# Kernel optimization log

Measured on AMD Instinct MI355X. Metric: run time of the kernel, lower is better.

Reference implementation:

```python
import jax, jax.numpy as jnp
import numpy as np

NUM_REL = 20000
NUM_EDGES = 640000
DIM_IN = 128
DIM_OUT = 128
NUM_HEAD = 8
DIM_HID = DIM_OUT // NUM_HEAD
NUM_BIN = 10
NEG_SLOPE = 0.2


def leaky_relu(x):
    return jnp.where(x >= 0, x, NEG_SLOPE * x)


def setup_inputs() -> dict:
    key = jax.random.key(0)
    ks = jax.random.split(key, 8)
    emb_rel = jax.random.normal(ks[0], (NUM_REL, DIM_IN), dtype=jnp.float32)
    head = jax.random.randint(ks[1], (NUM_EDGES, 1), 0, NUM_REL)
    tail = jax.random.randint(ks[2], (NUM_EDGES, 1), 0, NUM_REL)
    bins = jax.random.randint(ks[3], (NUM_EDGES, 1), 0, NUM_BIN)
    relation_triplets = jnp.concatenate([head, tail, bins], axis=-1).astype(jnp.int64)
    # xavier-normal-ish init
    attn_proj_w = jax.random.normal(ks[4], (DIM_OUT, 2 * DIM_IN), dtype=jnp.float32) * (2.0 / np.sqrt(2 * DIM_IN + DIM_OUT))
    attn_proj_b = jnp.zeros((DIM_OUT,), dtype=jnp.float32)
    attn_bin = jax.random.normal(ks[5], (NUM_BIN, NUM_HEAD, 1), dtype=jnp.float32) * 0.3
    attn_vec = jax.random.normal(ks[6], (1, NUM_HEAD, DIM_HID), dtype=jnp.float32) * (2.0 / np.sqrt(NUM_HEAD * DIM_HID))
    aggr_proj_w = jax.random.normal(ks[7], (DIM_OUT, DIM_IN), dtype=jnp.float32) * (2.0 / np.sqrt(DIM_IN + DIM_OUT))
    aggr_proj_b = jnp.zeros((DIM_OUT,), dtype=jnp.float32)
    return {"emb_rel": emb_rel, "relation_triplets": relation_triplets,
            "attn_proj_w": attn_proj_w, "attn_proj_b": attn_proj_b,
            "attn_bin": attn_bin, "attn_vec": attn_vec,
            "aggr_proj_w": aggr_proj_w, "aggr_proj_b": aggr_proj_b}


def reference(emb_rel, relation_triplets, attn_proj_w, attn_proj_b, attn_bin, attn_vec, aggr_proj_w, aggr_proj_b):
    num_rel = emb_rel.shape[0]
    head = relation_triplets[..., 0]
    tail = relation_triplets[..., 1]
    bins = relation_triplets[..., 2]
    # edge gather + concat: [E, 2*dim_in]
    concat = jnp.concatenate([emb_rel[head], emb_rel[tail]], axis=-1)
    proj = concat @ attn_proj_w.T + attn_proj_b  # [E, dim_out]
    proj = leaky_relu(proj).reshape(-1, NUM_HEAD, DIM_HID)
    attn_raw = (proj * attn_vec).sum(axis=-1, keepdims=True) + leaky_relu(attn_bin[bins])  # [E,H,1]
    # per-head-relation segment softmax over edges grouped by head index
    seg_max = jax.ops.segment_max(attn_raw, head, num_segments=num_rel)  # [R,H,1]
    attn_val = jnp.exp(attn_raw - seg_max[head])
    seg_sum = jax.ops.segment_sum(attn_val, head, num_segments=num_rel)  # [R,H,1]
    beta = attn_val / (seg_sum[head] + 1e-16)
    msg = (emb_rel[tail] @ aggr_proj_w.T + aggr_proj_b).reshape(-1, NUM_HEAD, DIM_HID)
    out = jax.ops.segment_sum(beta * msg, head, num_segments=num_rel)  # [R,H,Dh]
    return out.reshape(num_rel, -1)
```

## Files before the change

kernel.cpp:

```cpp
#include <hip/hip_runtime.h>
#include <hip/hip_bf16.h>
#include <cstdint>
#include <cstddef>

#define NUM_REL    20000
#define NUM_EDGES  640000
#define DIM        128
#define NUM_HEAD   8
#define DIM_HID    16
#define NUM_BIN    10
#define CAP        128
#define CNT_STR    16
#define PROJ_BLKS  471
#define SC_BLKS    1250

using u16 = unsigned short;
using u32 = unsigned int;
typedef __attribute__((ext_vector_type(8))) short bf16x8;
typedef __attribute__((ext_vector_type(4))) float f32x4;

__device__ __forceinline__ float b2f(u16 u) { return __uint_as_float(((u32)u) << 16); }
__device__ __forceinline__ float lo2f(u32 u) { return __uint_as_float(u << 16); }
__device__ __forceinline__ float hi2f(u32 u) { return __uint_as_float(u & 0xffff0000u); }
__device__ __forceinline__ float lrelu(float x) { return fmaxf(x, 0.2f * x); }
__device__ __forceinline__ int clampi(int v, int hi) { return v < 0 ? 0 : (v > hi ? hi : v); }
__device__ __forceinline__ float ldf(const void* p, int f32m, int i)
{ return f32m ? ((const float*)p)[i] : b2f(((const u16*)p)[i]); }
__device__ __forceinline__ u16 f2b(float x)
{ u32 u = __float_as_uint(x); u += 0x7fffu + ((u >> 16) & 1u); return (u16)(u >> 16); }
__device__ __forceinline__ u32 pk2(float a, float b)
{ return (u32)f2b(a) | ((u32)f2b(b) << 16); }

__device__ __forceinline__ void detect_flags(const int* __restrict__ trip,
                                             const u16* __restrict__ emb,
                                             int* sF, int tid)
{
    if (tid < 64) {
        bool odd_zero = (trip[2 * tid + 1] == 0) && (trip[2 * tid + 129] == 0);
        unsigned long long m1 = __ballot(odd_zero);
        int ex = (emb[2 * tid] >> 7) & 0xFF;
        bool inr = (ex >= 110) && (ex <= 136);
        unsigned long long m2 = __ballot(inr);
        if (tid == 0) {
            sF[0] = (~m1 == 0ull) ? 1 : 0;
            sF[1] = (__popcll(m2) >= 32) ? 0 : 1;
        }
    }
    __syncthreads();
}

__global__ __launch_bounds__(256) void k_projscatter(
    const void* __restrict__ emb, const int* __restrict__ trip,
    const void* __restrict__ w_attn, const void* __restrict__ w_aggr,
    const void* __restrict__ b_attn, const void* __restrict__ b_aggr,
    float* __restrict__ A, u16* __restrict__ Bb, u16* __restrict__ Mb,
    int* __restrict__ cnt, int* __restrict__ bucket)
{
    __shared__ u16 sW[128 * 64];
    __shared__ float sBias[128];
    __shared__ int sF[2];

    const int tid = threadIdx.x;
    detect_flags(trip, (const u16*)emb, sF, tid);
    const int is64 = sF[0], f32m = sF[1];

    if (blockIdx.x >= PROJ_BLKS) {
        int e0 = (blockIdx.x - PROJ_BLKS) * 512 + tid;
        int e1 = e0 + 256;
        int h0, t0, b0, h1, t1, b1;
        if (is64) {
            int2 ha = *(const int2*)(trip + 6 * e0);
            int2 ta = *(const int2*)(trip + 6 * e0 + 2);
            int2 ba = *(const int2*)(trip + 6 * e0 + 4);
            int2 hb = *(const int2*)(trip + 6 * e1);
            int2 tb = *(const int2*)(trip + 6 * e1 + 2);
            int2 bb = *(const int2*)(trip + 6 * e1 + 4);
            h0 = ha.x; t0 = ta.x; b0 = ba.x;
            h1 = hb.x; t1 = tb.x; b1 = bb.x;
        } else {
            h0 = trip[3 * e0]; t0 = trip[3 * e0 + 1]; b0 = trip[3 * e0 + 2];
            h1 = trip[3 * e1]; t1 = trip[3 * e1 + 1]; b1 = trip[3 * e1 + 2];
        }
        h0 = clampi(h0, NUM_REL - 1); t0 = clampi(t0, NUM_REL - 1); b0 = clampi(b0, NUM_BIN - 1);
        h1 = clampi(h1, NUM_REL - 1); t1 = clampi(t1, NUM_REL - 1); b1 = clampi(b1, NUM_BIN - 1);
        int p0 = atomicAdd(&cnt[h0 * CNT_STR], 1);
        int p1 = atomicAdd(&cnt[h1 * CNT_STR], 1);
        if (p0 < CAP) bucket[h0 * CAP + p0] = t0 | (b0 << 20);
        if (p1 < CAP) bucket[h1 * CAP + p1] = t1 | (b1 << 20);
        return;
    }

    const int mt = blockIdx.x / 3, nt = blockIdx.x % 3;
    const int r0 = mt * 128;

    if (tid < 128)
        sBias[tid] = (nt == 0) ? 0.f : ldf((nt == 1) ? b_attn : b_aggr, f32m, tid);

    const void* wsrc = (nt == 2) ? w_aggr : w_attn;
    const int stride = (nt == 2) ? 128 : 256;
    const int koff   = (nt == 1) ? 128 : 0;

    const int lane = tid & 63, wid = tid >> 6;
    const int wm = (wid >> 1) * 64, wn = (wid & 1) * 64;
    const int ln15 = lane & 15, q = lane >> 4;

    int arow[4];
    #pragma unroll
    for (int mi = 0; mi < 4; ++mi) {
        int g = r0 + wm + mi * 16 + ln15;
        arow[mi] = (g < NUM_REL) ? g : (NUM_REL - 1);
    }

    f32x4 acc[4][4] = {};
    #pragma unroll
    for (int kh = 0; kh < 2; ++kh) {
        if (kh) __syncthreads();
        if (f32m) {
            const float* src = (const float*)wsrc;
            #pragma unroll
            for (int i = 0; i < 8; ++i) {
                int f = i * 256 + tid;
                int row = f >> 4, pos = f & 15;
                const float* rp = src + (size_t)row * stride + koff + kh * 64;
                float4 x = ((const float4*)rp)[pos];
                int chunk = (pos >> 1) ^ (row & 7);
                *(uint2*)&sW[row * 64 + chunk * 8 + (pos & 1) * 4] =
                    make_uint2(pk2(x.x, x.y), pk2(x.z, x.w));
            }
        } else {
            const u16* src = (const u16*)wsrc;
            #pragma unroll
            for (int i = 0; i < 4; ++i) {
                int f = i * 256 + tid;
                int row = f >> 3, pos = f & 7;
                const u16* rp = src + (size_t)row * stride + koff + kh * 64;
                uint4 x = ((const uint4*)rp)[pos];
                int chunk = pos ^ (row & 7);
                *(uint4*)&sW[row * 64 + chunk * 8] = x;
            }
        }
        __syncthreads();

        #pragma unroll
        for (int k2 = 0; k2 < 2; ++k2) {
            const int kkg = kh * 2 + k2;
            const int kc = (kkg * 4 + q) * 8;
            const int cl = (k2 * 4 + q) ^ (ln15 & 7);
            bf16x8 a[4], b[4];
            #pragma unroll
            for (int mi = 0; mi < 4; ++mi) {
                if (f32m) {
                    const float* er = (const float*)emb + (size_t)arow[mi] * DIM + kc;
                    float4 x0 = *(const float4*)er;
                    float4 x1 = *(const float4*)(er + 4);
                    union { bf16x8 v; u32 u[4]; } cv;
                    cv.u[0] = pk2(x0.x, x0.y); cv.u[1] = pk2(x0.z, x0.w);
                    cv.u[2] = pk2(x1.x, x1.y); cv.u[3] = pk2(x1.z, x1.w);
                    a[mi] = cv.v;
                } else {
                    a[mi] = *(const bf16x8*)((const u16*)emb + (size_t)arow[mi] * DIM + kc);
                }
            }
            #pragma unroll
            for (int ni = 0; ni < 4; ++ni) {
                int n = wn + ni * 16 + ln15;
                b[ni] = *(const bf16x8*)&sW[n * 64 + cl * 8];
            }
            #pragma unroll
            for (int mi = 0; mi < 4; ++mi)
                #pragma unroll
                for (int ni = 0; ni < 4; ++ni)
                    acc[mi][ni] = __builtin_amdgcn_mfma_f32_16x16x32_bf16(
                        a[mi], b[ni], acc[mi][ni], 0, 0, 0);
        }
    }

    #pragma unroll
    for (int mi = 0; mi < 4; ++mi) {
        #pragma unroll
        for (int reg = 0; reg < 4; ++reg) {
            int g = r0 + wm + mi * 16 + q * 4 + reg;
            if (g < NUM_REL) {
                #pragma unroll
                for (int ni = 0; ni < 4; ++ni) {
                    int c = wn + ni * 16 + ln15;
                    float v = acc[mi][ni][reg] + sBias[c];
                    size_t o = (size_t)g * DIM + c;
                    if (nt == 0)      A[o]  = v;
                    else if (nt == 1) Bb[o] = f2b(v);
                    else              Mb[o] = f2b(v);
                }
            }
        }
    }
}

__global__ __launch_bounds__(256, 4) void k_segment(
    const float* __restrict__ A, const u16* __restrict__ Bb,
    const u16* __restrict__ Mb, const void* __restrict__ attn_bin,
    const void* __restrict__ attn_vec, const int* __restrict__ cnt,
    const int* __restrict__ bucket, const int* __restrict__ trip,
    const void* __restrict__ emb, void* __restrict__ out)
{
    __shared__ float sAr[4][DIM];
    __shared__ float sVec[DIM];
    __shared__ float sBin[NUM_BIN * NUM_HEAD];
    __shared__ int sF[2];

    const int tid  = threadIdx.x;
    detect_flags(trip, (const u16*)emb, sF, tid);
    const int f32m = sF[1];

    const int wid  = tid >> 6, lane = tid & 63;
    const int r = blockIdx.x * 4 + wid;
    int nE = cnt[r * CNT_STR]; if (nE > CAP) nE = CAP;
    const int* __restrict__ bk = bucket + r * CAP;

    {
        const float2* ap = (const float2*)(A + (size_t)r * DIM);
        float2 a2 = ap[lane];
        sAr[wid][2 * lane] = a2.x; sAr[wid][2 * lane + 1] = a2.y;
    }
    if (tid < DIM) sVec[tid] = ldf(attn_vec, f32m, tid);
    else if (tid < DIM + NUM_BIN * NUM_HEAD)
        sBin[tid - DIM] = lrelu(ldf(attn_bin, f32m, tid - DIM));
    __syncthreads();

    if (nE == 0) {
        if (f32m) ((float2*)out)[(size_t)r * 64 + lane] = make_float2(0.f, 0.f);
        else      ((u32*)out)[(size_t)r * 64 + lane] = 0;
        return;
    }

    const int el = lane >> 3, hd = lane & 7;
    const int ah = lane >> 3;

    float av[16], vv[16];
    {
        const float4* pA = (const float4*)(&sAr[wid][hd * DIM_HID]);
        const float4* pV = (const float4*)(&sVec[hd * DIM_HID]);
        #pragma unroll
        for (int i = 0; i < 4; ++i) {
            float4 a4 = pA[i], v4 = pV[i];
            av[4*i+0]=a4.x; av[4*i+1]=a4.y; av[4*i+2]=a4.z; av[4*i+3]=a4.w;
            vv[4*i+0]=v4.x; vv[4*i+1]=v4.y; vv[4*i+2]=v4.z; vv[4*i+3]=v4.w;
        }
    }

    const u16* __restrict__ Mbl = Mb + 2 * lane;

    int tba = (el      < nE) ? bk[el]     : 0;
    int tbb = (8 + el  < nE) ? bk[8 + el] : 0;
    int ia = tba & 0xFFFFF, ib = tbb & 0xFFFFF;
    uint4 q0a, q1a, q0b, q1b;
    {
        const uint4* Ba = (const uint4*)(Bb + (size_t)ia * DIM) + hd * 2;
        const uint4* Bc = (const uint4*)(Bb + (size_t)ib * DIM) + hd * 2;
        q0a = Ba[0]; q1a = Ba[1];
        q0b = Bc[0]; q1b = Bc[1];
    }

    float l = 0.f;
    float ax0 = 0.f, ax1 = 0.f, ay0 = 0.f, ay1 = 0.f;

    for (int base = 0; base < nE; base += 16) {
        u32 mm[16];
        #pragma unroll
        for (int k = 0; k < 8; ++k) {
            int tk = __shfl(ia, k * 8);
            mm[k] = *(const u32*)(Mbl + (size_t)tk * DIM);
        }
        #pragma unroll
        for (int k = 0; k < 8; ++k) {
            int tk = __shfl(ib, k * 8);
            mm[8 + k] = *(const u32*)(Mbl + (size_t)tk * DIM);
        }
        const int bsa = (tba >> 20) & 0xF;
        const int bsb = (tbb >> 20) & 0xF;

        int ea_n  = base + 16 + el;
        int eb_n  = base + 24 + el;
        int tba_n = (ea_n < nE) ? bk[ea_n] : 0;
        int tbb_n = (eb_n < nE) ? bk[eb_n] : 0;
        int ia_n  = tba_n & 0xFFFFF, ib_n = tbb_n & 0xFFFFF;
        uint4 q0an, q1an, q0bn, q1bn;
        {
            const uint4* Ban = (const uint4*)(Bb + (size_t)ia_n * DIM) + hd * 2;
            const uint4* Bcn = (const uint4*)(Bb + (size_t)ib_n * DIM) + hd * 2;
            q0an = Ban[0]; q1an = Ban[1];
            q0bn = Bcn[0]; q1bn = Bcn[1];
        }

        float sa0 = sBin[bsa * NUM_HEAD + hd];
        float sb0 = sBin[bsb * NUM_HEAD + hd];
        sa0 = fmaf(lrelu(av[0]  + lo2f(q0a.x)), vv[0],  sa0);
        sb0 = fmaf(lrelu(av[0]  + lo2f(q0b.x)), vv[0],  sb0);
        float sa1 = lrelu(av[1] + hi2f(q0a.x)) * vv[1];
        float sb1 = lrelu(av[1] + hi2f(q0b.x)) * vv[1];
        float sa2 = lrelu(av[2] + lo2f(q0a.y)) * vv[2];
        float sb2 = lrelu(av[2] + lo2f(q0b.y)) * vv[2];
        float sa3 = lrelu(av[3] + hi2f(q0a.y)) * vv[3];
        float sb3 = lrelu(av[3] + hi2f(q0b.y)) * vv[3];
        sa0 = fmaf(lrelu(av[4]  + lo2f(q0a.z)), vv[4],  sa0);
        sb0 = fmaf(lrelu(av[4]  + lo2f(q0b.z)), vv[4],  sb0);
        sa1 = fmaf(lrelu(av[5]  + hi2f(q0a.z)), vv[5],  sa1);
        sb1 = fmaf(lrelu(av[5]  + hi2f(q0b.z)), vv[5],  sb1);
        sa2 = fmaf(lrelu(av[6]  + lo2f(q0a.w)), vv[6],  sa2);
        sb2 = fmaf(lrelu(av[6]  + lo2f(q0b.w)), vv[6],  sb2);
        sa3 = fmaf(lrelu(av[7]  + hi2f(q0a.w)), vv[7],  sa3);
        sb3 = fmaf(lrelu(av[7]  + hi2f(q0b.w)), vv[7],  sb3);
        sa0 = fmaf(lrelu(av[8]  + lo2f(q1a.x)), vv[8],  sa0);
        sb0 = fmaf(lrelu(av[8]  + lo2f(q1b.x)), vv[8],  sb0);
        sa1 = fmaf(lrelu(av[9]  + hi2f(q1a.x)), vv[9],  sa1);
        sb1 = fmaf(lrelu(av[9]  + hi2f(q1b.x)), vv[9],  sb1);
        sa2 = fmaf(lrelu(av[10] + lo2f(q1a.y)), vv[10], sa2);
        sb2 = fmaf(lrelu(av[10] + lo2f(q1b.y)), vv[10], sb2);
        sa3 = fmaf(lrelu(av[11] + hi2f(q1a.y)), vv[11], sa3);
        sb3 = fmaf(lrelu(av[11] + hi2f(q1b.y)), vv[11], sb3);
        sa0 = fmaf(lrelu(av[12] + lo2f(q1a.z)), vv[12], sa0);
        sb0 = fmaf(lrelu(av[12] + lo2f(q1b.z)), vv[12], sb0);
        sa1 = fmaf(lrelu(av[13] + hi2f(q1a.z)), vv[13], sa1);
        sb1 = fmaf(lrelu(av[13] + hi2f(q1b.z)), vv[13], sb1);
        sa2 = fmaf(lrelu(av[14] + lo2f(q1a.w)), vv[14], sa2);
        sb2 = fmaf(lrelu(av[14] + lo2f(q1b.w)), vv[14], sb2);
        sa3 = fmaf(lrelu(av[15] + hi2f(q1a.w)), vv[15], sa3);
        sb3 = fmaf(lrelu(av[15] + hi2f(q1b.w)), vv[15], sb3);
        float sa = (sa0 + sa1) + (sa2 + sa3);
        float sb = (sb0 + sb1) + (sb2 + sb3);
        sa = fminf(fmaxf(sa, -60.f), 60.f);
        sb = fminf(fmaxf(sb, -60.f), 60.f);
        float pa = ((base + el)     < nE) ? __expf(sa) : 0.f;
        float pb = ((base + 8 + el) < nE) ? __expf(sb) : 0.f;
        l += pa + pb;

        #pragma unroll
        for (int k = 0; k < 8; ++k) {
            float v = __shfl(pa, k * 8 + ah);
            if (k & 1) { ax1 = fmaf(v, lo2f(mm[k]), ax1); ay1 = fmaf(v, hi2f(mm[k]), ay1); }
            else       { ax0 = fmaf(v, lo2f(mm[k]), ax0); ay0 = fmaf(v, hi2f(mm[k]), ay0); }
        }
        #pragma unroll
        for (int k = 0; k < 8; ++k) {
            float v = __shfl(pb, k * 8 + ah);
            if (k & 1) { ax1 = fmaf(v, lo2f(mm[8+k]), ax1); ay1 = fmaf(v, hi2f(mm[8+k]), ay1); }
            else       { ax0 = fmaf(v, lo2f(mm[8+k]), ax0); ay0 = fmaf(v, hi2f(mm[8+k]), ay0); }
        }

        tba = tba_n; tbb = tbb_n; ia = ia_n; ib = ib_n;
        q0a = q0an; q1a = q1an; q0b = q0bn; q1b = q1bn;
    }

    float accx = ax0 + ax1, accy = ay0 + ay1;

    float lt = l + __shfl_xor(l, 8);
    lt += __shfl_xor(lt, 16);
    lt += __shfl_xor(lt, 32);
    float lA = __shfl(lt, ah);
    float inv = 1.0f / (lA + 1e-16f);
    float o0 = accx * inv, o1 = accy * inv;
    if (f32m) {
        ((float2*)out)[(size_t)r * 64 + lane] = make_float2(o0, o1);
    } else {
        u32 pk = (u32)f2b(o0) | ((u32)f2b(o1) << 16);
        ((u32*)out)[(size_t)r * 64 + lane] = pk;
    }
}

extern "C" void kernel_launch(void* const* d_in, const int* in_sizes, int n_in,
                              void* d_out, int out_size, void* d_ws, size_t ws_size,
                              hipStream_t stream)
{
    (void)in_sizes; (void)n_in; (void)out_size; (void)ws_size;
    const void* emb      = d_in[0];
    const int*  trip     = (const int*)d_in[1];
    const void* w_attn   = d_in[2];
    const void* b_attn   = d_in[3];
    const void* attn_bin = d_in[4];
    const void* attn_vec = d_in[5];
    const void* w_aggr   = d_in[6];
    const void* b_aggr   = d_in[7];

    char* p = (char*)d_ws;
    float* A      = (float*)p; p += (size_t)NUM_REL * DIM * 4;
    u16*   Bb     = (u16*)p;   p += (size_t)NUM_REL * DIM * 2;
    u16*   Mb     = (u16*)p;   p += (size_t)NUM_REL * DIM * 2;
    int*   bucket = (int*)p;   p += (size_t)NUM_REL * CAP * 4;
    int*   cnt    = (int*)p;   p += (size_t)NUM_REL * CNT_STR * 4;

    hipMemsetAsync(cnt, 0, (size_t)NUM_REL * CNT_STR * sizeof(int), stream);
    k_projscatter<<<PROJ_BLKS + SC_BLKS, 256, 0, stream>>>(
        emb, trip, w_attn, w_aggr, b_attn, b_aggr, A, Bb, Mb, cnt, bucket);
    k_segment<<<NUM_REL / 4, 256, 0, stream>>>(A, Bb, Mb, attn_bin, attn_vec,
                                               cnt, bucket, trip, emb, d_out);
}
```

Baseline: 162.9 us.

## Split scatter from projection kernel, vectorize triplet loads, stage full-K weights once

The fused projection-plus-scatter kernel is split into two launches. The scatter kernel now handles four edges per thread and reads the triplets with wide int4 loads, so it issues more atomics per thread and needs fewer blocks. The projection kernel loads the full 128-wide K slice of the weights into LDS once, using a 16-way XOR swizzle, which removes the second weight load and the extra barrier. The costs are an extra kernel launch, the loss of overlap between scatter and GEMM blocks inside one grid, and double the LDS per block, which may lower occupancy.

```diff
diff --git a/kernel.cpp b/kernel.cpp
--- a/kernel.cpp
+++ b/kernel.cpp
@@ -12,7 +12,7 @@
 #define CAP        128
 #define CNT_STR    16
 #define PROJ_BLKS  471
-#define SC_BLKS    1250
+#define SCAT_BLKS  625
 
 using u16 = unsigned short;
 using u32 = unsigned int;
@@ -49,46 +49,58 @@
     __syncthreads();
 }
 
-__global__ __launch_bounds__(256) void k_projscatter(
+__global__ __launch_bounds__(256) void k_scatter(
+    const int* __restrict__ trip, const void* __restrict__ emb,
+    int* __restrict__ cnt, int* __restrict__ bucket)
+{
+    __shared__ int sF[2];
+    const int tid = threadIdx.x;
+    detect_flags(trip, (const u16*)emb, sF, tid);
+    const int is64 = sF[0];
+
+    const int e0 = (blockIdx.x * 256 + tid) * 4;
+    int h[4], t[4], b[4], p[4];
+    if (is64) {
+        const int4* w = (const int4*)(trip + 6 * e0);
+        int4 w0 = w[0], w1 = w[1], w2 = w[2], w3 = w[3], w4 = w[4], w5 = w[5];
+        h[0] = w0.x; t[0] = w0.z; b[0] = w1.x;
+        h[1] = w1.z; t[1] = w2.x; b[1] = w2.z;
+        h[2] = w3.x; t[2] = w3.z; b[2] = w4.x;
+        h[3] = w4.z; t[3] = w5.x; b[3] = w5.z;
+    } else {
+        const int4* w = (const int4*)(trip + 3 * e0);
+        int4 w0 = w[0], w1 = w[1], w2 = w[2];
+        h[0] = w0.x; t[0] = w0.y; b[0] = w0.z;
+        h[1] = w0.w; t[1] = w1.x; b[1] = w1.y;
+        h[2] = w1.z; t[2] = w1.w; b[2] = w2.x;
+        h[3] = w2.y; t[3] = w2.z; b[3] = w2.w;
+    }
+    #pragma unroll
+    for (int i = 0; i < 4; ++i) {
+        h[i] = clampi(h[i], NUM_REL - 1);
+        t[i] = clampi(t[i], NUM_REL - 1);
+        b[i] = clampi(b[i], NUM_BIN - 1);
+    }
+    #pragma unroll
+    for (int i = 0; i < 4; ++i) p[i] = atomicAdd(&cnt[h[i] * CNT_STR], 1);
+    #pragma unroll
+    for (int i = 0; i < 4; ++i)
+        if (p[i] < CAP) bucket[h[i] * CAP + p[i]] = t[i] | (b[i] << 20);
+}
+
+__global__ __launch_bounds__(256) void k_proj(
     const void* __restrict__ emb, const int* __restrict__ trip,
     const void* __restrict__ w_attn, const void* __restrict__ w_aggr,
     const void* __restrict__ b_attn, const void* __restrict__ b_aggr,
-    float* __restrict__ A, u16* __restrict__ Bb, u16* __restrict__ Mb,
-    int* __restrict__ cnt, int* __restrict__ bucket)
+    float* __restrict__ A, u16* __restrict__ Bb, u16* __restrict__ Mb)
 {
-    __shared__ u16 sW[128 * 64];
+    __shared__ u16 sW[128 * 128];
     __shared__ float sBias[128];
     __shared__ int sF[2];
 
     const int tid = threadIdx.x;
     detect_flags(trip, (const u16*)emb, sF, tid);
-    const int is64 = sF[0], f32m = sF[1];
-
-    if (blockIdx.x >= PROJ_BLKS) {
-        int e0 = (blockIdx.x - PROJ_BLKS) * 512 + tid;
-        int e1 = e0 + 256;
-        int h0, t0, b0, h1, t1, b1;
-        if (is64) {
-            int2 ha = *(const int2*)(trip + 6 * e0);
-            int2 ta = *(const int2*)(trip + 6 * e0 + 2);
-            int2 ba = *(const int2*)(trip + 6 * e0 + 4);
-            int2 hb = *(const int2*)(trip + 6 * e1);
-            int2 tb = *(const int2*)(trip + 6 * e1 + 2);
-            int2 bb = *(const int2*)(trip + 6 * e1 + 4);
-            h0 = ha.x; t0 = ta.x; b0 = ba.x;
-            h1 = hb.x; t1 = tb.x; b1 = bb.x;
-        } else {
-            h0 = trip[3 * e0]; t0 = trip[3 * e0 + 1]; b0 = trip[3 * e0 + 2];
-            h1 = trip[3 * e1]; t1 = trip[3 * e1 + 1]; b1 = trip[3 * e1 + 2];
-        }
-        h0 = clampi(h0, NUM_REL - 1); t0 = clampi(t0, NUM_REL - 1); b0 = clampi(b0, NUM_BIN - 1);
-        h1 = clampi(h1, NUM_REL - 1); t1 = clampi(t1, NUM_REL - 1); b1 = clampi(b1, NUM_BIN - 1);
-        int p0 = atomicAdd(&cnt[h0 * CNT_STR], 1);
-        int p1 = atomicAdd(&cnt[h1 * CNT_STR], 1);
-        if (p0 < CAP) bucket[h0 * CAP + p0] = t0 | (b0 << 20);
-        if (p1 < CAP) bucket[h1 * CAP + p1] = t1 | (b1 << 20);
-        return;
-    }
+    const int f32m = sF[1];
 
     const int mt = blockIdx.x / 3, nt = blockIdx.x % 3;
     const int r0 = mt * 128;
@@ -96,83 +108,78 @@
     if (tid < 128)
         sBias[tid] = (nt == 0) ? 0.f : ldf((nt == 1) ? b_attn : b_aggr, f32m, tid);
 
-    const void* wsrc = (nt == 2) ? w_aggr : w_attn;
-    const int stride = (nt == 2) ? 128 : 256;
-    const int koff   = (nt == 1) ? 128 : 0;
-
-    const int lane = tid & 63, wid = tid >> 6;
-    const int wm = (wid >> 1) * 64, wn = (wid & 1) * 64;
-    const int ln15 = lane & 15, q = lane >> 4;
-
-    int arow[4];
-    #pragma unroll
-    for (int mi = 0; mi < 4; ++mi) {
-        int g = r0 + wm + mi * 16 + ln15;
-        arow[mi] = (g < NUM_REL) ? g : (NUM_REL - 1);
-    }
-
-    f32x4 acc[4][4] = {};
-    #pragma unroll
-    for (int kh = 0; kh < 2; ++kh) {
-        if (kh) __syncthreads();
+    {
+        const void* wsrc = (nt == 2) ? w_aggr : w_attn;
+        const int stride = (nt == 2) ? 128 : 256;
+        const int koff   = (nt == 1) ? 128 : 0;
         if (f32m) {
             const float* src = (const float*)wsrc;
             #pragma unroll
-            for (int i = 0; i < 8; ++i) {
+            for (int i = 0; i < 16; ++i) {
                 int f = i * 256 + tid;
-                int row = f >> 4, pos = f & 15;
-                const float* rp = src + (size_t)row * stride + koff + kh * 64;
-                float4 x = ((const float4*)rp)[pos];
-                int chunk = (pos >> 1) ^ (row & 7);
-                *(uint2*)&sW[row * 64 + chunk * 8 + (pos & 1) * 4] =
+                int row = f >> 5, pos = f & 31;
+                float4 x = ((const float4*)(src + (size_t)row * stride + koff))[pos];
+                int chunk = (pos >> 1) ^ (row & 15);
+                *(uint2*)&sW[row * 128 + chunk * 8 + (pos & 1) * 4] =
                     make_uint2(pk2(x.x, x.y), pk2(x.z, x.w));
             }
         } else {
             const u16* src = (const u16*)wsrc;
             #pragma unroll
-            for (int i = 0; i < 4; ++i) {
+            for (int i = 0; i < 8; ++i) {
                 int f = i * 256 + tid;
-                int row = f >> 3, pos = f & 7;
-                const u16* rp = src + (size_t)row * stride + koff + kh * 64;
-                uint4 x = ((const uint4*)rp)[pos];
-                int chunk = pos ^ (row & 7);
-                *(uint4*)&sW[row * 64 + chunk * 8] = x;
+                int row = f >> 4, pos = f & 15;
+                uint4 x = ((const uint4*)(src + (size_t)row * stride + koff))[pos];
+                int chunk = pos ^ (row & 15);
+                *(uint4*)&sW[row * 128 + chunk * 8] = x;
             }
         }
-        __syncthreads();
-
-        #pragma unroll
-        for (int k2 = 0; k2 < 2; ++k2) {
-            const int kkg = kh * 2 + k2;
-            const int kc = (kkg * 4 + q) * 8;
-            const int cl = (k2 * 4 + q) ^ (ln15 & 7);
-            bf16x8 a[4], b[4];
+    }
+    __syncthreads();
+
+    const int lane = tid & 63, wid = tid >> 6;
+    const int wm = (wid >> 1) * 64, wn = (wid & 1) * 64;
+    const int ln15 = lane & 15, q = lane >> 4;
+
+    int arow[4];
+    #pragma unroll
+    for (int mi = 0; mi < 4; ++mi) {
+        int g = r0 + wm + mi * 16 + ln15;
+        arow[mi] = (g < NUM_REL) ? g : (NUM_REL - 1);
+    }
+
+    f32x4 acc[4][4] = {};
+    #pragma unroll
+    for (int kk = 0; kk < 4; ++kk) {
+        const int cbase = kk * 4 + q;
+        const int kc = cbase * 8;
+        bf16x8 a[4], b[4];
+        #pragma unroll
+        for (int mi = 0; mi < 4; ++mi) {
+            if (f32m) {
+                const float* er = (const float*)emb + (size_t)arow[mi] * DIM + kc;
+                float4 x0 = *(const float4*)er;
+                float4 x1 = *(const float4*)(er + 4);
+                union { bf16x8 v; u32 u[4]; } cv;
+                cv.u[0] = pk2(x0.x, x0.y); cv.u[1] = pk2(x0.z, x0.w);
+                cv.u[2] = pk2(x1.x, x1.y); cv.u[3] = pk2(x1.z, x1.w);
+                a[mi] = cv.v;
+            } else {
+                a[mi] = *(const bf16x8*)((const u16*)emb + (size_t)arow[mi] * DIM + kc);
+            }
+        }
+        #pragma unroll
+        for (int ni = 0; ni < 4; ++ni) {
+            int n = wn + ni * 16 + ln15;
+            int c = cbase ^ ln15;
+            b[ni] = *(const bf16x8*)&sW[n * 128 + c * 8];
+        }
+        #pragma unroll
+        for (int mi = 0; mi < 4; ++mi)
             #pragma unroll
-            for (int mi = 0; mi < 4; ++mi) {
-                if (f32m) {
-                    const float* er = (const float*)emb + (size_t)arow[mi] * DIM + kc;
-                    float4 x0 = *(const float4*)er;
-                    float4 x1 = *(const float4*)(er + 4);
-                    union { bf16x8 v; u32 u[4]; } cv;
-                    cv.u[0] = pk2(x0.x, x0.y); cv.u[1] = pk2(x0.z, x0.w);
-                    cv.u[2] = pk2(x1.x, x1.y); cv.u[3] = pk2(x1.z, x1.w);
-                    a[mi] = cv.v;
-                } else {
-                    a[mi] = *(const bf16x8*)((const u16*)emb + (size_t)arow[mi] * DIM + kc);
-                }
-            }
-            #pragma unroll
-            for (int ni = 0; ni < 4; ++ni) {
-                int n = wn + ni * 16 + ln15;
-                b[ni] = *(const bf16x8*)&sW[n * 64 + cl * 8];
-            }
-            #pragma unroll
-            for (int mi = 0; mi < 4; ++mi)
-                #pragma unroll
-                for (int ni = 0; ni < 4; ++ni)
-                    acc[mi][ni] = __builtin_amdgcn_mfma_f32_16x16x32_bf16(
-                        a[mi], b[ni], acc[mi][ni], 0, 0, 0);
-        }
+            for (int ni = 0; ni < 4; ++ni)
+                acc[mi][ni] = __builtin_amdgcn_mfma_f32_16x16x32_bf16(
+                    a[mi], b[ni], acc[mi][ni], 0, 0, 0);
     }
 
     #pragma unroll
@@ -388,8 +395,9 @@
     int*   cnt    = (int*)p;   p += (size_t)NUM_REL * CNT_STR * 4;
 
     hipMemsetAsync(cnt, 0, (size_t)NUM_REL * CNT_STR * sizeof(int), stream);
-    k_projscatter<<<PROJ_BLKS + SC_BLKS, 256, 0, stream>>>(
-        emb, trip, w_attn, w_aggr, b_attn, b_aggr, A, Bb, Mb, cnt, bucket);
+    k_scatter<<<SCAT_BLKS, 256, 0, stream>>>(trip, emb, cnt, bucket);
+    k_proj<<<PROJ_BLKS, 256, 0, stream>>>(
+        emb, trip, w_attn, w_aggr, b_attn, b_aggr, A, Bb, Mb);
     k_segment<<<NUM_REL / 4, 256, 0, stream>>>(A, Bb, Mb, attn_bin, attn_vec,
                                                cnt, bucket, trip, emb, d_out);
 }
```

After: 169.4 us. +4.0%, slower.
